# Performance work log

Measured on AMD Instinct MI355X. Metric: run time of the kernel, lower is better.

Reference implementation:

```python
import jax, jax.numpy as jnp
import numpy as np

GAMMA = 0.2
P = 3
N = 16384


def setup_inputs() -> dict:
    key = jax.random.key(0)
    k1, k2 = jax.random.split(key)
    y_pred = jax.random.normal(k1, (N, 2), dtype=jnp.float32)
    y_true = jax.random.randint(k2, (N,), 0, 2, dtype=jnp.int32)
    return {"y_pred": y_pred, "y_true": y_true}


def reference(y_pred, y_true):
    # softmax over classes, take probability of class 1 -> [N]
    s = jax.nn.softmax(y_pred, axis=-1)[:, 1]
    pos_mask = (y_true == 1)
    neg_mask = ~pos_mask
    # difference[j, i] = pos_i - neg_j - gamma  (rows: negatives, cols: positives)
    diff = s[None, :] - s[:, None] - GAMMA  # [N, N]
    pair = neg_mask[:, None] & pos_mask[None, :]
    valid = pair & (diff < 0.0)
    # sum of (-diff)^p over masked entries == hinge^p penalty
    contrib = jnp.where(valid, (-diff) ** P, jnp.zeros_like(diff))
    return jnp.sum(contrib)
```

## Files before the change

### kernel.cpp

```cpp
#include <hip/hip_runtime.h>
#include <math.h>

#define GAMMA_F 0.2f
#define NT 256
#define MAXLEN 1024

__device__ __forceinline__ float sigmoid_from_logits(float y0, float y1) {
    return 1.0f / (1.0f + __expf(y0 - y1));
}

__global__ __launch_bounds__(NT) void fused_pair_kernel(
        const float* __restrict__ y_pred, const int* __restrict__ y_true,
        int n, int len, float* __restrict__ partials) {
    __shared__ float row_a[NT];
    __shared__ float col_s[MAXLEN + 4];
    __shared__ int cnts[2];
    __shared__ float wsum[NT / 64];

    int tid = threadIdx.x;
    int lane = tid & 63;
    unsigned long long lt = (1ULL << lane) - 1ULL;
    if (tid < 2) cnts[tid] = 0;
    __syncthreads();

    {
        int i = blockIdx.x * NT + tid;
        bool in = (i < n);
        float a = 0.0f;
        bool is_pos = false;
        if (in) {
            float2 y = ((const float2*)y_pred)[i];
            a = sigmoid_from_logits(y.x, y.y) - GAMMA_F;
            is_pos = (y_true[i] == 1);
        }
        unsigned long long m = __ballot(is_pos);
        int base = 0;
        if (lane == 0) base = atomicAdd(&cnts[0], __popcll(m));
        base = __shfl(base, 0, 64);
        if (is_pos) row_a[base + __popcll(m & lt)] = a;
    }

    int j0 = blockIdx.y * len;
    int j1 = min(n, j0 + len);
    for (int c = j0; c < j1; c += NT) {
        int j = c + tid;
        bool in = (j < j1);
        float s = 0.0f;
        bool is_neg = false;
        if (in) {
            float2 y = ((const float2*)y_pred)[j];
            s = sigmoid_from_logits(y.x, y.y);
            is_neg = (y_true[j] != 1);
        }
        unsigned long long m = __ballot(is_neg);
        int base = 0;
        if (lane == 0) base = atomicAdd(&cnts[1], __popcll(m));
        base = __shfl(base, 0, 64);
        if (is_neg) col_s[base + __popcll(m & lt)] = s;
    }
    __syncthreads();

    int n_rows = cnts[0];
    int n_cols = cnts[1];

    int half = (n_cols / 2) & ~3;
    int p = tid & 1;
    int c0 = p ? half : 0;
    int c1 = p ? n_cols : half;
    int c4len = (c1 - c0) & ~3;

    float acc0 = 0.0f, acc1 = 0.0f, acc2 = 0.0f, acc3 = 0.0f;
    for (int r = tid >> 1; r < n_rows; r += NT / 2) {
        float av = row_a[r];
        int c = c0;
        int c4end = c0 + c4len;
        for (; c < c4end; c += 4) {
            float4 b = *(const float4*)&col_s[c];
            float t0 = fmaxf(b.x - av, 0.0f);
            float t1 = fmaxf(b.y - av, 0.0f);
            float t2 = fmaxf(b.z - av, 0.0f);
            float t3 = fmaxf(b.w - av, 0.0f);
            acc0 += (t0 * t0) * t0;
            acc1 += (t1 * t1) * t1;
            acc2 += (t2 * t2) * t2;
            acc3 += (t3 * t3) * t3;
        }
        for (; c < c1; ++c) {
            float t = fmaxf(col_s[c] - av, 0.0f);
            acc0 += (t * t) * t;
        }
    }
    float acc = (acc0 + acc1) + (acc2 + acc3);

    #pragma unroll
    for (int off = 32; off > 0; off >>= 1) acc += __shfl_down(acc, off, 64);
    int wave = tid >> 6;
    if (lane == 0) wsum[wave] = acc;
    __syncthreads();
    if (tid == 0) {
        float s = 0.0f;
        #pragma unroll
        for (int w = 0; w < NT / 64; ++w) s += wsum[w];
        partials[blockIdx.y * gridDim.x + blockIdx.x] = s;
    }
}

__global__ __launch_bounds__(NT) void reduce_kernel(
        const float* __restrict__ partials, int nb, float* __restrict__ out) {
    int tid = threadIdx.x;
    float s = 0.0f;
    for (int k = tid; k < nb; k += NT) s += partials[k];
    #pragma unroll
    for (int off = 32; off > 0; off >>= 1) s += __shfl_down(s, off, 64);
    __shared__ float wsum[NT / 64];
    int wave = tid >> 6, lane = tid & 63;
    if (lane == 0) wsum[wave] = s;
    __syncthreads();
    if (tid == 0) {
        float t = 0.0f;
        #pragma unroll
        for (int w = 0; w < NT / 64; ++w) t += wsum[w];
        out[0] = t;
    }
}

extern "C" void kernel_launch(void* const* d_in, const int* in_sizes, int n_in,
                              void* d_out, int out_size, void* d_ws, size_t ws_size,
                              hipStream_t stream) {
    const float* y_pred = (const float*)d_in[0];
    const int* y_true = (const int*)d_in[1];
    int n = in_sizes[1];
    float* out = (float*)d_out;

    int gx = (n + NT - 1) / NT;
    int nsplit = (n + MAXLEN - 1) / MAXLEN;
    int len = (n + nsplit - 1) / nsplit;
    int nb = gx * nsplit;

    float* partials = (float*)d_ws;

    dim3 grid(gx, nsplit);
    fused_pair_kernel<<<grid, NT, 0, stream>>>(y_pred, y_true, n, len, partials);
    reduce_kernel<<<1, NT, 0, stream>>>(partials, nb, out);
}
```

Baseline: 70.73 us.

## Register-block 4 rows per thread over 1024x1024 tiles, reduce atomically

Result: faster. 64.11 us (-9.4%).

```diff
diff --git a/kernel.cpp b/kernel.cpp
--- a/kernel.cpp
+++ b/kernel.cpp
@@ -2,8 +2,8 @@
 #include <math.h>
 
 #define GAMMA_F 0.2f
-#define NT 256
-#define MAXLEN 1024
+#define NT 1024
+#define NPART 16
 
 __device__ __forceinline__ float sigmoid_from_logits(float y0, float y1) {
     return 1.0f / (1.0f + __expf(y0 - y1));
@@ -11,9 +11,9 @@
 
 __global__ __launch_bounds__(NT) void fused_pair_kernel(
         const float* __restrict__ y_pred, const int* __restrict__ y_true,
-        int n, int len, float* __restrict__ partials) {
-    __shared__ float row_a[NT];
-    __shared__ float col_s[MAXLEN + 4];
+        int n, float* __restrict__ out) {
+    __shared__ float row_a[NT + 4];
+    __shared__ float col_s[NT + 4];
     __shared__ int cnts[2];
     __shared__ float wsum[NT / 64];
 
@@ -39,12 +39,9 @@
         base = __shfl(base, 0, 64);
         if (is_pos) row_a[base + __popcll(m & lt)] = a;
     }
-
-    int j0 = blockIdx.y * len;
-    int j1 = min(n, j0 + len);
-    for (int c = j0; c < j1; c += NT) {
-        int j = c + tid;
-        bool in = (j < j1);
+    {
+        int j = blockIdx.y * NT + tid;
+        bool in = (j < n);
         float s = 0.0f;
         bool is_neg = false;
         if (in) {
@@ -62,32 +59,42 @@
 
     int n_rows = cnts[0];
     int n_cols = cnts[1];
+    if (tid < 4) {
+        row_a[n_rows + tid] = 1e30f;
+        col_s[n_cols + tid] = -1e30f;
+    }
+    __syncthreads();
 
-    int half = (n_cols / 2) & ~3;
-    int p = tid & 1;
-    int c0 = p ? half : 0;
-    int c1 = p ? n_cols : half;
-    int c4len = (c1 - c0) & ~3;
+    int p = tid & (NPART - 1);
+    int g = tid >> 4;
+    int nf4 = (n_cols + 3) >> 2;
+    const float4* col4 = (const float4*)col_s;
 
     float acc0 = 0.0f, acc1 = 0.0f, acc2 = 0.0f, acc3 = 0.0f;
-    for (int r = tid >> 1; r < n_rows; r += NT / 2) {
-        float av = row_a[r];
-        int c = c0;
-        int c4end = c0 + c4len;
-        for (; c < c4end; c += 4) {
-            float4 b = *(const float4*)&col_s[c];
-            float t0 = fmaxf(b.x - av, 0.0f);
-            float t1 = fmaxf(b.y - av, 0.0f);
-            float t2 = fmaxf(b.z - av, 0.0f);
-            float t3 = fmaxf(b.w - av, 0.0f);
-            acc0 += (t0 * t0) * t0;
-            acc1 += (t1 * t1) * t1;
-            acc2 += (t2 * t2) * t2;
-            acc3 += (t3 * t3) * t3;
-        }
-        for (; c < c1; ++c) {
-            float t = fmaxf(col_s[c] - av, 0.0f);
-            acc0 += (t * t) * t;
+    for (int r = g * 4; r < n_rows; r += (NT / NPART) * 4) {
+        float a0 = row_a[r + 0];
+        float a1 = row_a[r + 1];
+        float a2 = row_a[r + 2];
+        float a3 = row_a[r + 3];
+        for (int k = p; k < nf4; k += NPART) {
+            float4 b = col4[k];
+            float t;
+            t = fmaxf(b.x - a0, 0.0f); acc0 += (t * t) * t;
+            t = fmaxf(b.x - a1, 0.0f); acc1 += (t * t) * t;
+            t = fmaxf(b.x - a2, 0.0f); acc2 += (t * t) * t;
+            t = fmaxf(b.x - a3, 0.0f); acc3 += (t * t) * t;
+            t = fmaxf(b.y - a0, 0.0f); acc0 += (t * t) * t;
+            t = fmaxf(b.y - a1, 0.0f); acc1 += (t * t) * t;
+            t = fmaxf(b.y - a2, 0.0f); acc2 += (t * t) * t;
+            t = fmaxf(b.y - a3, 0.0f); acc3 += (t * t) * t;
+            t = fmaxf(b.z - a0, 0.0f); acc0 += (t * t) * t;
+            t = fmaxf(b.z - a1, 0.0f); acc1 += (t * t) * t;
+            t = fmaxf(b.z - a2, 0.0f); acc2 += (t * t) * t;
+            t = fmaxf(b.z - a3, 0.0f); acc3 += (t * t) * t;
+            t = fmaxf(b.w - a0, 0.0f); acc0 += (t * t) * t;
+            t = fmaxf(b.w - a1, 0.0f); acc1 += (t * t) * t;
+            t = fmaxf(b.w - a2, 0.0f); acc2 += (t * t) * t;
+            t = fmaxf(b.w - a3, 0.0f); acc3 += (t * t) * t;
         }
     }
     float acc = (acc0 + acc1) + (acc2 + acc3);
@@ -101,26 +108,7 @@
         float s = 0.0f;
         #pragma unroll
         for (int w = 0; w < NT / 64; ++w) s += wsum[w];
-        partials[blockIdx.y * gridDim.x + blockIdx.x] = s;
-    }
-}
-
-__global__ __launch_bounds__(NT) void reduce_kernel(
-        const float* __restrict__ partials, int nb, float* __restrict__ out) {
-    int tid = threadIdx.x;
-    float s = 0.0f;
-    for (int k = tid; k < nb; k += NT) s += partials[k];
-    #pragma unroll
-    for (int off = 32; off > 0; off >>= 1) s += __shfl_down(s, off, 64);
-    __shared__ float wsum[NT / 64];
-    int wave = tid >> 6, lane = tid & 63;
-    if (lane == 0) wsum[wave] = s;
-    __syncthreads();
-    if (tid == 0) {
-        float t = 0.0f;
-        #pragma unroll
-        for (int w = 0; w < NT / 64; ++w) t += wsum[w];
-        out[0] = t;
+        atomicAdd(out, s);
     }
 }
 
@@ -131,15 +119,9 @@
     const int* y_true = (const int*)d_in[1];
     int n = in_sizes[1];
     float* out = (float*)d_out;
+    (void)d_ws; (void)ws_size;
 
-    int gx = (n + NT - 1) / NT;
-    int nsplit = (n + MAXLEN - 1) / MAXLEN;
-    int len = (n + nsplit - 1) / nsplit;
-    int nb = gx * nsplit;
-
-    float* partials = (float*)d_ws;
-
-    dim3 grid(gx, nsplit);
-    fused_pair_kernel<<<grid, NT, 0, stream>>>(y_pred, y_true, n, len, partials);
-    reduce_kernel<<<1, NT, 0, stream>>>(partials, nb, out);
+    int g = (n + NT - 1) / NT;
+    dim3 grid(g, g), block(NT);
+    fused_pair_kernel<<<grid, block, 0, stream>>>(y_pred, y_true, n, out);
 }
```
